# Kernel optimization log

Measured on AMD Instinct MI355X. Metric: run time of the kernel, lower is better.

Reference implementation:

```python
import jax, jax.numpy as jnp
import numpy as np

DIM = 1024
SEQ = 4096


def setup_inputs() -> dict:
    key = jax.random.key(0)
    ks = jax.random.split(key, 7)
    s = 1.0 / np.sqrt(DIM)
    return {
        "X": jax.random.normal(ks[0], (SEQ, DIM), dtype=jnp.float32),
        "Wq": jax.random.uniform(ks[1], (DIM, DIM), jnp.float32, -s, s),
        "bq": jax.random.uniform(ks[2], (DIM,), jnp.float32, -s, s),
        "Wk": jax.random.uniform(ks[3], (DIM, DIM), jnp.float32, -s, s),
        "bk": jax.random.uniform(ks[4], (DIM,), jnp.float32, -s, s),
        "Wv": jax.random.uniform(ks[5], (DIM, DIM), jnp.float32, -s, s),
        "bv": jax.random.uniform(ks[6], (DIM,), jnp.float32, -s, s),
    }


def reference(X, Wq, bq, Wk, bk, Wv, bv):
    # QKV projections (nn.Linear: x @ W.T + b); here W stored as [in, out]
    Q = X @ Wq + bq            # [S, D]
    K = X @ Wk + bk            # [S, D]
    V = X @ Wv + bv            # [S, D]
    scale = 1.0 / jnp.sqrt(jnp.asarray(X.shape[-1], X.dtype))
    scores = (Q @ K.T) * scale  # [S, S]
    attn = jax.nn.softmax(scores, axis=-1)
    return attn @ V            # [S, D]
```

## Files before the change

kernel.cpp:

```cpp
#include <hip/hip_runtime.h>

typedef unsigned short u16;
typedef unsigned int u32;
typedef __bf16 bf16x8 __attribute__((ext_vector_type(8)));
typedef float f32x4 __attribute__((ext_vector_type(4)));
typedef u16 u16x4 __attribute__((ext_vector_type(4)));

__device__ __forceinline__ u16 f32_to_bf16(float f) {
    u32 u = __builtin_bit_cast(u32, f);
    u32 r = (u + 0x7fffu + ((u >> 16) & 1u)) >> 16;
    return (u16)r;
}

__device__ __forceinline__ float bf16_to_f32(u16 h) {
    u32 u = (u32)h << 16;
    return __builtin_bit_cast(float, u);
}

__device__ __forceinline__ void async_cp16(const u16* g, u16* l) {
    __builtin_amdgcn_global_load_lds(
        (const __attribute__((address_space(1))) u32*)g,
        (__attribute__((address_space(3))) u32*)l, 16, 0, 0);
}

#define GEMM_PROLOG(Aptr, Bptr, LDA, LDB)                                     \
    __shared__ u16 lds[16384];                                                \
    const int tid  = threadIdx.x;                                             \
    const int wid  = tid >> 6;                                                \
    const int lane = tid & 63;                                                \
    const int s0 = wid * 2, s1 = s0 + 1;                                      \
    const int rr = lane >> 2;                                                 \
    const int cc = (lane & 3) * 8;                                            \
    const u16* gA0 = (Aptr) + (size_t)(bm + s0 * 16 + rr) * (LDA) + cc;       \
    const u16* gA1 = (Aptr) + (size_t)(bm + s1 * 16 + rr) * (LDA) + cc;      \
    const u16* gB0 = (Bptr) + (size_t)(bn + s0 * 16 + rr) * (LDB) + cc;       \
    const u16* gB1 = (Bptr) + (size_t)(bn + s1 * 16 + rr) * (LDB) + cc;       \
    u16* lA0  = &lds[s0 * 512];                                               \
    u16* lA1  = &lds[s1 * 512];                                               \
    u16* lA0h = lA0 + 4096;                                                   \
    u16* lA1h = lA1 + 4096;                                                   \
    u16* lB0  = &lds[8192 + s0 * 512];                                        \
    u16* lB1  = &lds[8192 + s1 * 512];                                        \
    u16* lB0h = lB0 + 4096;                                                   \
    u16* lB1h = lB1 + 4096;                                                   \
    const int wm = (wid >> 1) * 64;                                           \
    const int wn = (wid & 1) * 64;                                            \
    const int row16 = lane & 15;                                              \
    const int quad  = lane >> 4;                                              \
    f32x4 acc[4][4];                                                          \
    const f32x4 zero = {0.f, 0.f, 0.f, 0.f};                                  \
    _Pragma("unroll")                                                         \
    for (int i = 0; i < 4; i++)                                               \
        _Pragma("unroll")                                                     \
        for (int j = 0; j < 4; j++) acc[i][j] = zero;

#define GEMM_KLOOP(KLEN)                                                      \
    for (int kt = 0; kt < (KLEN); kt += 64) {                                 \
        __syncthreads();                                                      \
        async_cp16(gA0, lA0);                                                 \
        async_cp16(gA1, lA1);                                                 \
        async_cp16(gA0 + 32, lA0h);                                           \
        async_cp16(gA1 + 32, lA1h);                                           \
        async_cp16(gB0, lB0);                                                 \
        async_cp16(gB1, lB1);                                                 \
        async_cp16(gB0 + 32, lB0h);                                           \
        async_cp16(gB1 + 32, lB1h);                                           \
        gA0 += 64; gA1 += 64; gB0 += 64; gB1 += 64;                           \
        __syncthreads();                                                      \
        _Pragma("unroll")                                                     \
        for (int h = 0; h < 2; h++) {                                         \
            bf16x8 fa[4], fb[4];                                              \
            _Pragma("unroll")                                                 \
            for (int im = 0; im < 4; im++)                                    \
                fa[im] = *(const bf16x8*)&lds[h * 4096 + (wm + im * 16 + row16) * 32 + quad * 8]; \
            _Pragma("unroll")                                                 \
            for (int in = 0; in < 4; in++)                                    \
                fb[in] = *(const bf16x8*)&lds[8192 + h * 4096 + (wn + in * 16 + row16) * 32 + quad * 8]; \
            _Pragma("unroll")                                                 \
            for (int im = 0; im < 4; im++)                                    \
                _Pragma("unroll")                                             \
                for (int in = 0; in < 4; in++)                                \
                    acc[im][in] = __builtin_amdgcn_mfma_f32_16x16x32_bf16(    \
                        fa[im], fb[in], acc[im][in], 0, 0, 0);                \
        }                                                                     \
    }

#define SWIZZLE_2D()                                                          \
    const int L   = blockIdx.x;                                               \
    const int id2 = L & 255;                                                  \
    const int bm  = (((id2 & 7) * 4) + (id2 >> 6)) * 128;                     \
    const int bn  = (((id2 >> 3) & 7) + (L >> 8) * 8) * 128;

__global__ __launch_bounds__(256, 4)
void gemm_qkv(const u16* __restrict__ A, const u16* __restrict__ B,
              u16* __restrict__ C, u16* __restrict__ Vt,
              const float* __restrict__ bias,
              int K, int lda, int ldb, int ldc)
{
    SWIZZLE_2D()
    GEMM_PROLOG(A, B, lda, ldb)
    GEMM_KLOOP(K)
    if (bn < 2048) {
        #pragma unroll
        for (int im = 0; im < 4; im++) {
            #pragma unroll
            for (int in = 0; in < 4; in++) {
                const int n = bn + wn + in * 16 + row16;
                const float bv = bias[n];
                #pragma unroll
                for (int r = 0; r < 4; r++) {
                    const int m = bm + wm + im * 16 + quad * 4 + r;
                    C[(size_t)m * ldc + n] = f32_to_bf16(acc[im][in][r] + bv);
                }
            }
        }
    } else {
        #pragma unroll
        for (int im = 0; im < 4; im++) {
            #pragma unroll
            for (int in = 0; in < 4; in++) {
                const int n = bn + wn + in * 16 + row16;
                const float bv = bias[n];
                const int d = n - 2048;
                const int m = bm + wm + im * 16 + quad * 4;
                u16x4 pk;
                #pragma unroll
                for (int r = 0; r < 4; r++)
                    pk[r] = f32_to_bf16(acc[im][in][r] + bv);
                *(u16x4*)&Vt[(size_t)d * 4096 + m] = pk;
            }
        }
    }
}

__global__ __launch_bounds__(256, 4)
void gemm_score_exp(const u16* __restrict__ A, const u16* __restrict__ B,
                    u16* __restrict__ P, float* __restrict__ rowsum,
                    int K, int lda, int ldb, int ldc, float scale)
{
    SWIZZLE_2D()
    GEMM_PROLOG(A, B, lda, ldb)
    GEMM_KLOOP(K)
    #pragma unroll
    for (int im = 0; im < 4; im++) {
        #pragma unroll
        for (int r = 0; r < 4; r++) {
            const int m = bm + wm + im * 16 + quad * 4 + r;
            float rs = 0.f;
            #pragma unroll
            for (int in = 0; in < 4; in++) {
                const int n = bn + wn + in * 16 + row16;
                float e = __expf(acc[im][in][r] * scale);
                P[(size_t)m * ldc + n] = f32_to_bf16(e);
                rs += e;
            }
            rs += __shfl_xor(rs, 1);
            rs += __shfl_xor(rs, 2);
            rs += __shfl_xor(rs, 4);
            rs += __shfl_xor(rs, 8);
            if (row16 == 0) atomicAdd(&rowsum[m], rs);
        }
    }
}

__global__ __launch_bounds__(256, 4)
void gemm_pv_splitk(const u16* __restrict__ A, const u16* __restrict__ B,
                    float* __restrict__ out, const float* __restrict__ rowsum,
                    int Kq, int lda, int ldb)
{
    const int id2 = blockIdx.x;
    const int bm  = (((id2 & 7) * 4) + (id2 >> 6)) * 128;
    const int bn  = ((id2 >> 3) & 7) * 128;
    const int z   = blockIdx.y;
    const int koff = z * Kq;
    GEMM_PROLOG(A + koff, B + koff, lda, ldb)
    GEMM_KLOOP(Kq)
    #pragma unroll
    for (int im = 0; im < 4; im++) {
        #pragma unroll
        for (int r = 0; r < 4; r++) {
            const int m = bm + wm + im * 16 + quad * 4 + r;
            const float inv = 1.0f / rowsum[m];
            #pragma unroll
            for (int in = 0; in < 4; in++) {
                const int n = bn + wn + in * 16 + row16;
                atomicAdd(&out[(size_t)m * 1024 + n], acc[im][in][r] * inv);
            }
        }
    }
}

__global__ __launch_bounds__(256)
void prep_all(const float4* __restrict__ X, uint2* __restrict__ Xb,
              const float* __restrict__ W0, const float* __restrict__ W1,
              const float* __restrict__ W2, u16* __restrict__ Wt,
              const float* __restrict__ bq, const float* __restrict__ bk,
              const float* __restrict__ bv, float* __restrict__ b3,
              float* __restrict__ rowsum, float4* __restrict__ outz)
{
    __shared__ float t[32][33];
    const int b = blockIdx.x;
    if (b < 4096) {
        const int i = b * 256 + threadIdx.x;
        float4 v = X[i];
        uint2 o;
        o.x = (u32)f32_to_bf16(v.x) | ((u32)f32_to_bf16(v.y) << 16);
        o.y = (u32)f32_to_bf16(v.z) | ((u32)f32_to_bf16(v.w) << 16);
        Xb[i] = o;
    } else if (b < 7168) {
        const int tt = b - 4096;
        const int z  = tt >> 10;
        const int r  = tt & 1023;
        const float* W = (z == 0) ? W0 : (z == 1) ? W1 : W2;
        u16* dst = Wt + (size_t)z * 1024 * 1024;
        const int bk2 = (r & 31) * 32;
        const int bn2 = (r >> 5) * 32;
        const int tx = threadIdx.x & 31;
        const int ty = threadIdx.x >> 5;
        #pragma unroll
        for (int i = 0; i < 32; i += 8)
            t[ty + i][tx] = W[(size_t)(bk2 + ty + i) * 1024 + bn2 + tx];
        __syncthreads();
        #pragma unroll
        for (int i = 0; i < 32; i += 8)
            dst[(size_t)(bn2 + ty + i) * 1024 + bk2 + tx] = f32_to_bf16(t[tx][ty + i]);
    } else if (b < 7196) {
        const int i = (b - 7168) * 256 + threadIdx.x;
        if (i < 3072)
            b3[i] = (i < 1024) ? bq[i] : (i < 2048) ? bk[i - 1024] : bv[i - 2048];
        else
            rowsum[i - 3072] = 0.f;
    } else {
        const int i = (b - 7196) * 256 + threadIdx.x;
        const float4 z4 = {0.f, 0.f, 0.f, 0.f};
        outz[i] = z4;
    }
}

extern "C" void kernel_launch(void* const* d_in, const int* in_sizes, int n_in,
                              void* d_out, int out_size, void* d_ws, size_t ws_size,
                              hipStream_t stream)
{
    const float* X  = (const float*)d_in[0];
    const float* Wq = (const float*)d_in[1];
    const float* bq = (const float*)d_in[2];
    const float* Wk = (const float*)d_in[3];
    const float* bk = (const float*)d_in[4];
    const float* Wv = (const float*)d_in[5];
    const float* bv = (const float*)d_in[6];
    float* out = (float*)d_out;

    char* ws = (char*)d_ws;
    u16*   P      = (u16*)ws;
    u16*   Xb     = (u16*)ws;
    u16*   WqkvT  = (u16*)(ws + (8u << 20));
    float* rowsum = (float*)(ws + (32u << 20));
    float* bias3  = (float*)(ws + (32u << 20) + (64u << 10));
    u16*   QKV    = (u16*)(ws + (33u << 20));
    u16*   Vt     = (u16*)(ws + (65u << 20));

    prep_all<<<11292, 256, 0, stream>>>((const float4*)X, (uint2*)Xb,
        Wq, Wk, Wv, WqkvT, bq, bk, bv, bias3, rowsum, (float4*)out);

    gemm_qkv<<<768, 256, 0, stream>>>(Xb, WqkvT, QKV, Vt, bias3,
        1024, 1024, 1024, 3072);

    gemm_score_exp<<<1024, 256, 0, stream>>>(QKV, QKV + 1024, P, rowsum,
        1024, 3072, 3072, 4096, 0.03125f);

    gemm_pv_splitk<<<dim3(256, 4), 256, 0, stream>>>(P, Vt, out, rowsum,
        1024, 4096, 4096);
}
```

Measured before the change: 232.3 us.

## Replace split-K float atomics with bf16 partials and last-block reduction

The PV split-K kernel now writes each split's partial tile as bf16 into one of four workspace buffers instead of doing float atomicAdd into the output. A per-tile counter lets the last-arriving block sum the four partials, apply the softmax normalisation, and store the final fp32 tile with vector stores. This also removes the need to zero the output in the prep kernel, which now only resets the counters. The aim is to cut contended atomic traffic and the output memset. The cost is an extra bf16 rounding of partial sums, plus a fence and counter handshake per tile.

```diff
diff --git a/kernel.cpp b/kernel.cpp
--- a/kernel.cpp
+++ b/kernel.cpp
@@ -165,27 +165,60 @@
 
 __global__ __launch_bounds__(256, 4)
 void gemm_pv_splitk(const u16* __restrict__ A, const u16* __restrict__ B,
+                    u16* __restrict__ P0, u16* __restrict__ P1,
+                    u16* __restrict__ P2, u16* __restrict__ P3,
                     float* __restrict__ out, const float* __restrict__ rowsum,
-                    int Kq, int lda, int ldb)
-{
+                    u32* __restrict__ cnt,
+                    int Kq, int lda, int ldb, int ldc)
+{
+    __shared__ u32 lastflag;
     const int id2 = blockIdx.x;
     const int bm  = (((id2 & 7) * 4) + (id2 >> 6)) * 128;
     const int bn  = ((id2 >> 3) & 7) * 128;
     const int z   = blockIdx.y;
+    u16* C = (z == 0) ? P0 : (z == 1) ? P1 : (z == 2) ? P2 : P3;
     const int koff = z * Kq;
     GEMM_PROLOG(A + koff, B + koff, lda, ldb)
     GEMM_KLOOP(Kq)
     #pragma unroll
     for (int im = 0; im < 4; im++) {
         #pragma unroll
-        for (int r = 0; r < 4; r++) {
-            const int m = bm + wm + im * 16 + quad * 4 + r;
+        for (int in = 0; in < 4; in++) {
+            const int n = bn + wn + in * 16 + row16;
+            #pragma unroll
+            for (int r = 0; r < 4; r++) {
+                const int m = bm + wm + im * 16 + quad * 4 + r;
+                C[(size_t)m * ldc + n] = f32_to_bf16(acc[im][in][r]);
+            }
+        }
+    }
+    __threadfence();
+    __syncthreads();
+    if (tid == 0) lastflag = atomicAdd(&cnt[id2], 1u);
+    __syncthreads();
+    if (lastflag == 3u) {
+        __threadfence();
+        const u16x4* q0 = (const u16x4*)P0;
+        const u16x4* q1 = (const u16x4*)P1;
+        const u16x4* q2 = (const u16x4*)P2;
+        const u16x4* q3 = (const u16x4*)P3;
+        float4* o4p = (float4*)out;
+        const int bno4 = bn >> 2;
+        #pragma unroll 4
+        for (int it = 0; it < 16; it++) {
+            const int idx  = it * 256 + tid;
+            const int rowi = idx >> 5;
+            const int grp  = idx & 31;
+            const int m    = bm + rowi;
             const float inv = 1.0f / rowsum[m];
-            #pragma unroll
-            for (int in = 0; in < 4; in++) {
-                const int n = bn + wn + in * 16 + row16;
-                atomicAdd(&out[(size_t)m * 1024 + n], acc[im][in][r] * inv);
-            }
+            const size_t o4 = (size_t)m * 256 + bno4 + grp;
+            u16x4 a = q0[o4], b4 = q1[o4], c4 = q2[o4], d4 = q3[o4];
+            float4 o;
+            o.x = (bf16_to_f32(a[0]) + bf16_to_f32(b4[0]) + bf16_to_f32(c4[0]) + bf16_to_f32(d4[0])) * inv;
+            o.y = (bf16_to_f32(a[1]) + bf16_to_f32(b4[1]) + bf16_to_f32(c4[1]) + bf16_to_f32(d4[1])) * inv;
+            o.z = (bf16_to_f32(a[2]) + bf16_to_f32(b4[2]) + bf16_to_f32(c4[2]) + bf16_to_f32(d4[2])) * inv;
+            o.w = (bf16_to_f32(a[3]) + bf16_to_f32(b4[3]) + bf16_to_f32(c4[3]) + bf16_to_f32(d4[3])) * inv;
+            o4p[o4] = o;
         }
     }
 }
@@ -196,7 +229,7 @@
               const float* __restrict__ W2, u16* __restrict__ Wt,
               const float* __restrict__ bq, const float* __restrict__ bk,
               const float* __restrict__ bv, float* __restrict__ b3,
-              float* __restrict__ rowsum, float4* __restrict__ outz)
+              float* __restrict__ rowsum, u32* __restrict__ cnt)
 {
     __shared__ float t[32][33];
     const int b = blockIdx.x;
@@ -231,9 +264,7 @@
         else
             rowsum[i - 3072] = 0.f;
     } else {
-        const int i = (b - 7196) * 256 + threadIdx.x;
-        const float4 z4 = {0.f, 0.f, 0.f, 0.f};
-        outz[i] = z4;
+        cnt[threadIdx.x] = 0u;
     }
 }
 
@@ -255,12 +286,17 @@
     u16*   Xb     = (u16*)ws;
     u16*   WqkvT  = (u16*)(ws + (8u << 20));
     float* rowsum = (float*)(ws + (32u << 20));
+    u32*   cnt    = (u32*)(ws + (32u << 20) + (32u << 10));
     float* bias3  = (float*)(ws + (32u << 20) + (64u << 10));
     u16*   QKV    = (u16*)(ws + (33u << 20));
+    u16*   p0     = (u16*)(ws + (33u << 20));
+    u16*   p1     = (u16*)(ws + (41u << 20));
+    u16*   p2     = (u16*)(ws + (49u << 20));
+    u16*   p3     = (u16*)(ws + (57u << 20));
     u16*   Vt     = (u16*)(ws + (65u << 20));
 
-    prep_all<<<11292, 256, 0, stream>>>((const float4*)X, (uint2*)Xb,
-        Wq, Wk, Wv, WqkvT, bq, bk, bv, bias3, rowsum, (float4*)out);
+    prep_all<<<7197, 256, 0, stream>>>((const float4*)X, (uint2*)Xb,
+        Wq, Wk, Wv, WqkvT, bq, bk, bv, bias3, rowsum, cnt);
 
     gemm_qkv<<<768, 256, 0, stream>>>(Xb, WqkvT, QKV, Vt, bias3,
         1024, 1024, 1024, 3072);
@@ -268,6 +304,6 @@
     gemm_score_exp<<<1024, 256, 0, stream>>>(QKV, QKV + 1024, P, rowsum,
         1024, 3072, 3072, 4096, 0.03125f);
 
-    gemm_pv_splitk<<<dim3(256, 4), 256, 0, stream>>>(P, Vt, out, rowsum,
-        1024, 4096, 4096);
-}
+    gemm_pv_splitk<<<dim3(256, 4), 256, 0, stream>>>(P, Vt, p0, p1, p2, p3,
+        out, rowsum, cnt, 1024, 4096, 4096, 1024);
+}
```

Measured after the change: 378.1 us. +62.8%, slower.
